# Kernel tuning notes

Measured on AMD Instinct MI355X. Metric: run time of the kernel, lower is better.

Reference implementation:

```python
import jax, jax.numpy as jnp
import numpy as np

B, T, C = 2, 2048, 1024
H = 16
HD = C // H  # head_size = 64
FF = 2 * C   # ffwd_size default = n_embd * 2
EPS = float(jnp.finfo(jnp.float32).eps)  # torch RMSNorm eps=None -> finfo eps


def rmsnorm(x, g):
    # torch.nn.RMSNorm: x / sqrt(mean(x^2) + eps) * weight
    ms = jnp.mean(jnp.square(x), axis=-1, keepdims=True)
    return x * jax.lax.rsqrt(ms + EPS) * g


def setup_inputs() -> dict:
    key = jax.random.key(0)
    ks = jax.random.split(key, 12)
    s_in = 1.0 / np.sqrt(C)
    s_ff = 1.0 / np.sqrt(FF)
    return {
        "target": jax.random.normal(ks[0], (B, T, C), dtype=jnp.float32),
        # per-head projections, torch Linear layout [out, in] stacked over heads: [H, HD, C]
        "wq": jax.random.uniform(ks[1], (H, HD, C), jnp.float32, -s_in, s_in),
        "wk": jax.random.uniform(ks[2], (H, HD, C), jnp.float32, -s_in, s_in),
        "wv": jax.random.uniform(ks[3], (H, HD, C), jnp.float32, -s_in, s_in),
        "w_proj": jax.random.uniform(ks[4], (C, H * HD), jnp.float32, -s_in, s_in),
        "b_proj": jax.random.uniform(ks[5], (C,), jnp.float32, -s_in, s_in),
        "w1": jax.random.uniform(ks[6], (FF, C), jnp.float32, -s_in, s_in),
        "b1": jax.random.uniform(ks[7], (FF,), jnp.float32, -s_in, s_in),
        "w2": jax.random.uniform(ks[8], (C, FF), jnp.float32, -s_ff, s_ff),
        "b2": jax.random.uniform(ks[9], (C,), jnp.float32, -s_ff, s_ff),
        "g1": jnp.ones((C,), jnp.float32),
        "g2": jnp.ones((C,), jnp.float32),
    }


def reference(target, wq, wk, wv, w_proj, b_proj, w1, b1, w2, b2, g1, g2):
    x = rmsnorm(target, g1)
    # q,k,v: [B,H,T,HD]
    q = jnp.einsum("btc,hdc->bhtd", x, wq)
    k = jnp.einsum("btc,hdc->bhtd", x, wk)
    v = jnp.einsum("btc,hdc->bhtd", x, wv)
    scale = HD ** -0.5
    wei = jnp.einsum("bhtd,bhsd->bhts", q, k) * scale  # [B,H,T,T]
    causal = jnp.tril(jnp.ones((T, T), dtype=bool))
    wei = jnp.where(causal, wei, -jnp.inf)
    wei = jax.nn.softmax(wei, axis=-1)
    attn = jnp.einsum("bhts,bhsd->bhtd", wei, v)  # [B,H,T,HD]
    attn = attn.transpose(0, 2, 1, 3).reshape(B, T, H * HD)  # concat heads
    attn = attn @ w_proj.T + b_proj
    target = target + attn
    y = rmsnorm(target, g2)
    h = jax.nn.gelu(y @ w1.T + b1, approximate=False)  # torch nn.GELU default = exact
    ff = h @ w2.T + b2
    return target + ff
```

## Files before the change

kernel.cpp:

```cpp
#include <hip/hip_runtime.h>
#include <math.h>

#define B_  2
#define T_  2048
#define C_  1024
#define H_  16
#define HD_ 64
#define FF_ 2048
#define EPS_ 1.1920929e-07f

typedef __attribute__((ext_vector_type(8))) short short8;
typedef __attribute__((ext_vector_type(4))) float f32x4;

__device__ __forceinline__ unsigned short f2bf(float f) {
    unsigned u = __float_as_uint(f);
    u += 0x7fffu + ((u >> 16) & 1u);
    return (unsigned short)(u >> 16);
}
__device__ __forceinline__ float bf2f(unsigned short u) {
    return __uint_as_float(((unsigned)u) << 16);
}

__global__ void prep_kernel(const float* __restrict__ wq, const float* __restrict__ wk,
                            const float* __restrict__ wv, const float* __restrict__ wp,
                            const float* __restrict__ w1, const float* __restrict__ w2,
                            unsigned short* __restrict__ wb,
                            const float* __restrict__ x, const float* __restrict__ g,
                            unsigned short* __restrict__ y) {
    int tid = threadIdx.x;
    if (blockIdx.x < 8192) {
        size_t i = ((size_t)blockIdx.x * 256 + tid) * 4;
        const float* src; size_t off = i;
        if      (i < 1048576u)  { src = wq; }
        else if (i < 2097152u)  { src = wk; off = i - 1048576u; }
        else if (i < 3145728u)  { src = wv; off = i - 2097152u; }
        else if (i < 4194304u)  { src = wp; off = i - 3145728u; }
        else if (i < 6291456u)  { src = w1; off = i - 4194304u; }
        else                    { src = w2; off = i - 6291456u; }
        float4 v4 = *(const float4*)(src + off);
        ushort4 o4;
        o4.x = f2bf(v4.x); o4.y = f2bf(v4.y); o4.z = f2bf(v4.z); o4.w = f2bf(v4.w);
        *(ushort4*)(wb + i) = o4;
    } else {
        int row = blockIdx.x - 8192;
        const float4* xr = (const float4*)(x + (size_t)row * C_);
        float4 xv = xr[tid];
        float ss = xv.x * xv.x + xv.y * xv.y + xv.z * xv.z + xv.w * xv.w;
        #pragma unroll
        for (int m = 32; m >= 1; m >>= 1) ss += __shfl_xor(ss, m, 64);
        __shared__ float sred[4];
        if ((tid & 63) == 0) sred[tid >> 6] = ss;
        __syncthreads();
        float tot = sred[0] + sred[1] + sred[2] + sred[3];
        float r = rsqrtf(tot * (1.0f / C_) + EPS_);
        float4 gv = ((const float4*)g)[tid];
        ushort4 o;
        o.x = f2bf(xv.x * r * gv.x);
        o.y = f2bf(xv.y * r * gv.y);
        o.z = f2bf(xv.z * r * gv.z);
        o.w = f2bf(xv.w * r * gv.w);
        *((ushort4*)(y + (size_t)row * C_) + tid) = o;
    }
}

__global__ void rmsnorm_bf16_kernel(const float* __restrict__ x, const float* __restrict__ g,
                                    unsigned short* __restrict__ y) {
    int row = blockIdx.x;
    int tid = threadIdx.x;
    const float4* xr = (const float4*)(x + (size_t)row * C_);
    float4 xv = xr[tid];
    float ss = xv.x * xv.x + xv.y * xv.y + xv.z * xv.z + xv.w * xv.w;
    #pragma unroll
    for (int m = 32; m >= 1; m >>= 1) ss += __shfl_xor(ss, m, 64);
    __shared__ float sred[4];
    if ((tid & 63) == 0) sred[tid >> 6] = ss;
    __syncthreads();
    float tot = sred[0] + sred[1] + sred[2] + sred[3];
    float r = rsqrtf(tot * (1.0f / C_) + EPS_);
    float4 gv = ((const float4*)g)[tid];
    ushort4 o;
    o.x = f2bf(xv.x * r * gv.x);
    o.y = f2bf(xv.y * r * gv.y);
    o.z = f2bf(xv.z * r * gv.z);
    o.w = f2bf(xv.w * r * gv.w);
    *((ushort4*)(y + (size_t)row * C_) + tid) = o;
}

template <int TM, int ACT, bool BIAS, bool RES, bool OBF16, int ROUTE>
__global__ __launch_bounds__(256) void mfma_gemm(
        const unsigned short* __restrict__ A, const unsigned short* __restrict__ W,
        const float* __restrict__ bias, const float* __restrict__ resid,
        void* __restrict__ O0, void* __restrict__ O1, void* __restrict__ O2,
        int M, int N, int K) {
    constexpr int ACH = TM / 8;
    constexpr int NCH = (ACH + 16) / 4;
    constexpr int MI  = TM / 32;
    __shared__ short As[2 * TM * 32];
    __shared__ short Bs[2 * 128 * 32];
    const int tid  = threadIdx.x;
    const int w    = tid >> 6, lane = tid & 63;
    const int tileN = blockIdx.x * 128, tileM = blockIdx.y * TM;

    const unsigned short* gsrc[NCH];
    short* ldst[NCH];
    #pragma unroll
    for (int i2 = 0; i2 < NCH; ++i2) {
        int c = w * NCH + i2;
        if (c < ACH) {
            int kh = c / (ACH / 2), lc = c % (ACH / 2);
            gsrc[i2] = A + (size_t)(tileM + lc * 16 + (lane >> 2)) * K + kh * 32 + (lane & 3) * 8;
            ldst[i2] = As + c * 512;
        } else {
            int c2 = c - ACH;
            int kh = c2 >> 3, lc = c2 & 7;
            gsrc[i2] = W + (size_t)(tileN + lc * 16 + (lane >> 2)) * K + kh * 32 + (lane & 3) * 8;
            ldst[i2] = Bs + c2 * 512;
        }
    }

    f32x4 acc[MI][4];
    const f32x4 zed = {0.f, 0.f, 0.f, 0.f};
    #pragma unroll
    for (int i = 0; i < MI; ++i)
        #pragma unroll
        for (int j = 0; j < 4; ++j) acc[i][j] = zed;

    const int wm = (w >> 1) * (TM / 2), wn = (w & 1) * 64;
    const int frow = lane & 15, koff = (lane >> 4) * 8;

    for (int k0 = 0; k0 < K; k0 += 64) {
        #pragma unroll
        for (int i2 = 0; i2 < NCH; ++i2)
            __builtin_amdgcn_global_load_lds(
                (const __attribute__((address_space(1))) unsigned*)(gsrc[i2] + k0),
                (__attribute__((address_space(3))) unsigned*)ldst[i2], 16, 0, 0);
        __syncthreads();

        #pragma unroll
        for (int kh = 0; kh < 2; ++kh) {
            short8 af[MI], bfr[4];
            #pragma unroll
            for (int i = 0; i < MI; ++i)
                af[i] = *(const short8*)(As + kh * TM * 32 + (wm + i * 16 + frow) * 32 + koff);
            #pragma unroll
            for (int j = 0; j < 4; ++j)
                bfr[j] = *(const short8*)(Bs + kh * 128 * 32 + (wn + j * 16 + frow) * 32 + koff);
            #pragma unroll
            for (int i = 0; i < MI; ++i)
                #pragma unroll
                for (int j = 0; j < 4; ++j)
                    acc[i][j] = __builtin_amdgcn_mfma_f32_16x16x32_bf16(af[i], bfr[j], acc[i][j], 0, 0, 0);
        }
        __syncthreads();
    }

    const int ecol = lane & 15, erow = (lane >> 4) * 4;
    const int zone = ROUTE ? (tileN >> 10) : 0;
    #pragma unroll
    for (int j = 0; j < 4; ++j) {
        int n = tileN + wn + j * 16 + ecol;
        float bv = BIAS ? bias[n] : 0.f;
        int nl = ROUTE ? (n & 1023) : n;
        #pragma unroll
        for (int i = 0; i < MI; ++i) {
            int mbase = tileM + wm + i * 16 + erow;
            #pragma unroll
            for (int r = 0; r < 4; ++r) {
                float val = acc[i][j][r] + bv;
                if (ACT == 1) val = 0.5f * val * (1.0f + erff(val * 0.70710678118654752f));
                int mrow = mbase + r;
                if (ROUTE) {
                    if (zone == 0) {
                        ((unsigned short*)O0)[(size_t)mrow * 1024 + nl] = f2bf(val * 0.18033688011112042f);
                    } else if (zone == 1) {
                        ((unsigned short*)O1)[(size_t)mrow * 1024 + nl] = f2bf(val);
                    } else {
                        int bb = mrow >> 11, tt = mrow & 2047;
                        int hh = nl >> 6, dd = nl & 63;
                        ((unsigned short*)O2)[((size_t)((bb * 16 + hh) * 64 + dd)) * 2048 + tt] = f2bf(val);
                    }
                } else {
                    size_t idx = (size_t)mrow * N + n;
                    if (RES) val += resid[idx];
                    if (OBF16) ((unsigned short*)O0)[idx] = f2bf(val);
                    else       ((float*)O0)[idx] = val;
                }
            }
        }
    }
}

__global__ __launch_bounds__(256) void flash_mfma_kernel(
        const unsigned short* __restrict__ q, const unsigned short* __restrict__ k,
        const unsigned short* __restrict__ vT, unsigned short* __restrict__ out) {
    __shared__ unsigned short KsA[64 * 64];
    __shared__ unsigned short VtA[64 * 64];
    __shared__ unsigned short KsB[64 * 64];
    __shared__ unsigned short VtB[64 * 64];
    __shared__ unsigned short Ps[2 * 4 * 16 * 40];

    const int tid  = threadIdx.x;
    const int w    = tid >> 6, lane = tid & 63;
    const int quad = lane >> 4, l15 = lane & 15;
    const int bh = blockIdx.x;
    const int qt = (gridDim.y - 1) - blockIdx.y;
    const int h = bh & (H_ - 1);
    const int b = bh >> 4;

    const size_t qkbase = (size_t)b * T_ * C_ + h * HD_;
    const size_t vbase  = (size_t)(b * H_ + h) * HD_ * T_;

    short8 QB[2];
    {
        const unsigned short* qp = q + qkbase + (size_t)(qt * 64 + w * 16 + l15) * C_;
        QB[0] = *(const short8*)(qp + quad * 8);
        QB[1] = *(const short8*)(qp + 32 + quad * 8);
    }

    f32x4 O[4];
    const f32x4 zed = {0.f, 0.f, 0.f, 0.f};
    #pragma unroll
    for (int dt = 0; dt < 4; ++dt) O[dt] = zed;
    float l_i = 0.f;

    const int qg = qt * 64 + w * 16 + l15;
    const int psoff = w * 640 + l15 * 40;
    const int r8 = lane >> 3, c7 = lane & 7;
    const int cswz = (c7 ^ r8) * 8;
    const int swz15 = (l15 & 7);

    auto stageKV = [&](unsigned short* Ksb, unsigned short* Vtb, int st_) {
        const int s0_ = st_ * 64;
        #pragma unroll
        for (int c = 0; c < 2; ++c) {
            const int row = w * 16 + c * 8 + r8;
            const unsigned short* gk = k + qkbase + (size_t)(s0_ + row) * C_ + cswz;
            __builtin_amdgcn_global_load_lds(
                (const __attribute__((address_space(1))) unsigned*)gk,
                (__attribute__((address_space(3))) unsigned*)(Ksb + (w * 16 + c * 8) * 64), 16, 0, 0);
            const unsigned short* gv = vT + vbase + (size_t)row * T_ + s0_ + cswz;
            __builtin_amdgcn_global_load_lds(
                (const __attribute__((address_space(1))) unsigned*)gv,
                (__attribute__((address_space(3))) unsigned*)(Vtb + (w * 16 + c * 8) * 64), 16, 0, 0);
        }
    };

    auto computeTile = [&](const unsigned short* Ksb, const unsigned short* Vtb, int st_) {
        const bool diag = (st_ == qt);
        const int s0_ = st_ * 64;
        #pragma unroll
        for (int sb = 0; sb < 2; ++sb) {
            const int sbl = sb * 32;
            f32x4 Sacc[2];
            #pragma unroll
            for (int u = 0; u < 2; ++u) {
                const int row = sbl + 16 * u + l15;
                const unsigned short* kr = Ksb + row * 64;
                const int kc = (quad ^ swz15) * 8;
                short8 KA0 = *(const short8*)(kr + kc);
                short8 KA1 = *(const short8*)(kr + (kc ^ 32));
                Sacc[u] = __builtin_amdgcn_mfma_f32_16x16x32_bf16(KA0, QB[0], zed, 0, 0, 0);
                Sacc[u] = __builtin_amdgcn_mfma_f32_16x16x32_bf16(KA1, QB[1], Sacc[u], 0, 0, 0);
            }
            float vals[8];
            if (diag) {
                #pragma unroll
                for (int u = 0; u < 2; ++u)
                    #pragma unroll
                    for (int r = 0; r < 4; ++r) {
                        int sg = s0_ + sbl + 16 * u + quad * 4 + r;
                        vals[u * 4 + r] = (sg > qg) ? 0.f : __builtin_amdgcn_exp2f(Sacc[u][r]);
                    }
            } else {
                #pragma unroll
                for (int u = 0; u < 2; ++u)
                    #pragma unroll
                    for (int r = 0; r < 4; ++r)
                        vals[u * 4 + r] = __builtin_amdgcn_exp2f(Sacc[u][r]);
            }
            float rs = 0.f;
            #pragma unroll
            for (int i = 0; i < 8; ++i) rs += vals[i];
            rs += __shfl_xor(rs, 16, 64);
            rs += __shfl_xor(rs, 32, 64);
            l_i += rs;

            #pragma unroll
            for (int u = 0; u < 2; ++u) {
                uint2 pw;
                pw.x = (unsigned)f2bf(vals[u * 4 + 0]) | ((unsigned)f2bf(vals[u * 4 + 1]) << 16);
                pw.y = (unsigned)f2bf(vals[u * 4 + 2]) | ((unsigned)f2bf(vals[u * 4 + 3]) << 16);
                *(uint2*)&Ps[sb * 2560 + psoff + 16 * u + quad * 4] = pw;
            }
            __builtin_amdgcn_sched_barrier(0);

            short8 PA = *(const short8*)&Ps[sb * 2560 + psoff + quad * 8];
            __builtin_amdgcn_s_setprio(1);
            #pragma unroll
            for (int dt = 0; dt < 4; ++dt) {
                const int vrow = 16 * dt + l15;
                short8 VB = *(const short8*)(Vtb + vrow * 64 + (((4 * sb + quad) ^ swz15) * 8));
                O[dt] = __builtin_amdgcn_mfma_f32_16x16x32_bf16(PA, VB, O[dt], 0, 0, 0);
            }
            __builtin_amdgcn_s_setprio(0);
        }
    };

    stageKV(KsA, VtA, 0);
    __syncthreads();
    int st = 0;
    for (;;) {
        if (st + 1 <= qt) stageKV(KsB, VtB, st + 1);
        computeTile(KsA, VtA, st);
        __syncthreads();
        ++st; if (st > qt) break;
        if (st + 1 <= qt) stageKV(KsA, VtA, st + 1);
        computeTile(KsB, VtB, st);
        __syncthreads();
        ++st; if (st > qt) break;
    }

    f32x4 inv;
    #pragma unroll
    for (int r = 0; r < 4; ++r) inv[r] = 1.0f / __shfl(l_i, quad * 4 + r, 64);
    #pragma unroll
    for (int dt = 0; dt < 4; ++dt)
        #pragma unroll
        for (int r = 0; r < 4; ++r) {
            int row = qt * 64 + w * 16 + quad * 4 + r;
            int col = h * HD_ + dt * 16 + l15;
            out[((size_t)(b * T_ + row)) * C_ + col] = f2bf(O[dt][r] * inv[r]);
        }
}

extern "C" void kernel_launch(void* const* d_in, const int* in_sizes, int n_in,
                              void* d_out, int out_size, void* d_ws, size_t ws_size,
                              hipStream_t stream) {
    const float* target = (const float*)d_in[0];
    const float* wq     = (const float*)d_in[1];
    const float* wk     = (const float*)d_in[2];
    const float* wv     = (const float*)d_in[3];
    const float* w_proj = (const float*)d_in[4];
    const float* b_proj = (const float*)d_in[5];
    const float* w1     = (const float*)d_in[6];
    const float* b1     = (const float*)d_in[7];
    const float* w2     = (const float*)d_in[8];
    const float* b2     = (const float*)d_in[9];
    const float* g1     = (const float*)d_in[10];
    const float* g2     = (const float*)d_in[11];
    float* out = (float*)d_out;

    char* ws = (char*)d_ws;
    const size_t MB = 1u << 20;
    unsigned short* xn = (unsigned short*)(ws);
    unsigned short* q  = (unsigned short*)(ws + 8 * MB);
    unsigned short* k  = (unsigned short*)(ws + 16 * MB);
    unsigned short* vt = (unsigned short*)(ws + 24 * MB);
    float*          x2 = (float*)(ws + 32 * MB);
    unsigned short* wb = (unsigned short*)(ws + 48 * MB);
    unsigned short* y  = q;
    unsigned short* hb = k;

    unsigned short* wqkv_b = wb;
    unsigned short* wp_b   = wb + 3145728u;
    unsigned short* w1_b   = wb + 4194304u;
    unsigned short* w2_b   = wb + 6291456u;

    const int M = B_ * T_;

    prep_kernel<<<12288, 256, 0, stream>>>(wq, wk, wv, w_proj, w1, w2, wb, target, g1, xn);

    mfma_gemm<128, 0, false, false, true, 1><<<dim3(24, M / 128), 256, 0, stream>>>(
        xn, wqkv_b, nullptr, nullptr, q, k, vt, M, 3072, C_);

    flash_mfma_kernel<<<dim3(B_ * H_, T_ / 64), 256, 0, stream>>>(q, k, vt, xn);

    mfma_gemm<64, 0, true, true, false, 0><<<dim3(C_ / 128, M / 64), 256, 0, stream>>>(
        xn, wp_b, b_proj, target, x2, nullptr, nullptr, M, C_, C_);

    rmsnorm_bf16_kernel<<<M, 256, 0, stream>>>(x2, g2, y);

    mfma_gemm<64, 1, true, false, true, 0><<<dim3(FF_ / 128, M / 64), 256, 0, stream>>>(
        y, w1_b, b1, nullptr, hb, nullptr, nullptr, M, FF_, C_);

    mfma_gemm<64, 0, true, true, false, 0><<<dim3(C_ / 128, M / 64), 256, 0, stream>>>(
        hb, w2_b, b2, x2, out, nullptr, nullptr, M, C_, FF_);
}
```

Baseline: 279.8 us.

## Pair causal query tiles per block and merge S-subblock compute in flash attention

Each attention block now processes two query tiles, a short one (pair) and a long one (31-pair), so every block does a balanced amount of causal work and the grid halves to 32x16. The per-tile compute is also restructured to compute all four 16-row score fragments before a single exp/rowsum/P-store pass, then issue eight PV MFMAs, removing the intra-tile sched_barrier split. This targets tail imbalance from the causal triangle and gives more ILP per tile. The cost is fewer blocks, hence lower occupancy across CUs, higher register pressure from 16 live score values, and a block that runs two tiles back to back.

```diff
diff --git a/kernel.cpp b/kernel.cpp
--- a/kernel.cpp
+++ b/kernel.cpp
@@ -203,7 +203,7 @@
     const int w    = tid >> 6, lane = tid & 63;
     const int quad = lane >> 4, l15 = lane & 15;
     const int bh = blockIdx.x;
-    const int qt = (gridDim.y - 1) - blockIdx.y;
+    const int pair = blockIdx.y;
     const int h = bh & (H_ - 1);
     const int b = bh >> 4;
 
@@ -211,23 +211,16 @@
     const size_t vbase  = (size_t)(b * H_ + h) * HD_ * T_;
 
     short8 QB[2];
-    {
-        const unsigned short* qp = q + qkbase + (size_t)(qt * 64 + w * 16 + l15) * C_;
-        QB[0] = *(const short8*)(qp + quad * 8);
-        QB[1] = *(const short8*)(qp + 32 + quad * 8);
-    }
-
     f32x4 O[4];
     const f32x4 zed = {0.f, 0.f, 0.f, 0.f};
-    #pragma unroll
-    for (int dt = 0; dt < 4; ++dt) O[dt] = zed;
     float l_i = 0.f;
-
-    const int qg = qt * 64 + w * 16 + l15;
+    int qt = 0, qg = 0;
+
     const int psoff = w * 640 + l15 * 40;
     const int r8 = lane >> 3, c7 = lane & 7;
     const int cswz = (c7 ^ r8) * 8;
     const int swz15 = (l15 & 7);
+    const int kc = (quad ^ swz15) * 8;
 
     auto stageKV = [&](unsigned short* Ksb, unsigned short* Vtb, int st_) {
         const int s0_ = st_ * 64;
@@ -248,89 +241,96 @@
     auto computeTile = [&](const unsigned short* Ksb, const unsigned short* Vtb, int st_) {
         const bool diag = (st_ == qt);
         const int s0_ = st_ * 64;
-        #pragma unroll
-        for (int sb = 0; sb < 2; ++sb) {
-            const int sbl = sb * 32;
-            f32x4 Sacc[2];
-            #pragma unroll
-            for (int u = 0; u < 2; ++u) {
-                const int row = sbl + 16 * u + l15;
-                const unsigned short* kr = Ksb + row * 64;
-                const int kc = (quad ^ swz15) * 8;
-                short8 KA0 = *(const short8*)(kr + kc);
-                short8 KA1 = *(const short8*)(kr + (kc ^ 32));
-                Sacc[u] = __builtin_amdgcn_mfma_f32_16x16x32_bf16(KA0, QB[0], zed, 0, 0, 0);
-                Sacc[u] = __builtin_amdgcn_mfma_f32_16x16x32_bf16(KA1, QB[1], Sacc[u], 0, 0, 0);
+        f32x4 Sacc[4];
+        #pragma unroll
+        for (int i = 0; i < 4; ++i) {
+            const unsigned short* kr = Ksb + (i * 16 + l15) * 64;
+            short8 KA0 = *(const short8*)(kr + kc);
+            short8 KA1 = *(const short8*)(kr + (kc ^ 32));
+            Sacc[i] = __builtin_amdgcn_mfma_f32_16x16x32_bf16(KA0, QB[0], zed, 0, 0, 0);
+            Sacc[i] = __builtin_amdgcn_mfma_f32_16x16x32_bf16(KA1, QB[1], Sacc[i], 0, 0, 0);
+        }
+        float vals[16];
+        #pragma unroll
+        for (int i = 0; i < 4; ++i)
+            #pragma unroll
+            for (int r = 0; r < 4; ++r) {
+                float e = __builtin_amdgcn_exp2f(Sacc[i][r]);
+                if (diag) {
+                    int sg = s0_ + i * 16 + quad * 4 + r;
+                    e = (sg > qg) ? 0.f : e;
+                }
+                vals[i * 4 + r] = e;
             }
-            float vals[8];
-            if (diag) {
-                #pragma unroll
-                for (int u = 0; u < 2; ++u)
-                    #pragma unroll
-                    for (int r = 0; r < 4; ++r) {
-                        int sg = s0_ + sbl + 16 * u + quad * 4 + r;
-                        vals[u * 4 + r] = (sg > qg) ? 0.f : __builtin_amdgcn_exp2f(Sacc[u][r]);
-                    }
-            } else {
-                #pragma unroll
-                for (int u = 0; u < 2; ++u)
-                    #pragma unroll
-                    for (int r = 0; r < 4; ++r)
-                        vals[u * 4 + r] = __builtin_amdgcn_exp2f(Sacc[u][r]);
+        float rs = 0.f;
+        #pragma unroll
+        for (int i = 0; i < 16; ++i) rs += vals[i];
+        rs += __shfl_xor(rs, 16, 64);
+        rs += __shfl_xor(rs, 32, 64);
+        l_i += rs;
+
+        #pragma unroll
+        for (int i = 0; i < 4; ++i) {
+            const int sb = i >> 1, u = i & 1;
+            uint2 pw;
+            pw.x = (unsigned)f2bf(vals[i * 4 + 0]) | ((unsigned)f2bf(vals[i * 4 + 1]) << 16);
+            pw.y = (unsigned)f2bf(vals[i * 4 + 2]) | ((unsigned)f2bf(vals[i * 4 + 3]) << 16);
+            *(uint2*)&Ps[sb * 2560 + psoff + 16 * u + quad * 4] = pw;
+        }
+
+        short8 PA0 = *(const short8*)&Ps[psoff + quad * 8];
+        short8 PA1 = *(const short8*)&Ps[2560 + psoff + quad * 8];
+        __builtin_amdgcn_s_setprio(1);
+        #pragma unroll
+        for (int dt = 0; dt < 4; ++dt) {
+            const unsigned short* vr = Vtb + (16 * dt + l15) * 64;
+            short8 VB0 = *(const short8*)(vr + ((quad ^ swz15) * 8));
+            short8 VB1 = *(const short8*)(vr + (((4 + quad) ^ swz15) * 8));
+            O[dt] = __builtin_amdgcn_mfma_f32_16x16x32_bf16(PA0, VB0, O[dt], 0, 0, 0);
+            O[dt] = __builtin_amdgcn_mfma_f32_16x16x32_bf16(PA1, VB1, O[dt], 0, 0, 0);
+        }
+        __builtin_amdgcn_s_setprio(0);
+    };
+
+    #pragma unroll 1
+    for (int half = 0; half < 2; ++half) {
+        qt = half ? (T_ / 64 - 1 - pair) : pair;
+        qg = qt * 64 + w * 16 + l15;
+        {
+            const unsigned short* qp = q + qkbase + (size_t)(qt * 64 + w * 16 + l15) * C_;
+            QB[0] = *(const short8*)(qp + quad * 8);
+            QB[1] = *(const short8*)(qp + 32 + quad * 8);
+        }
+        #pragma unroll
+        for (int dt = 0; dt < 4; ++dt) O[dt] = zed;
+        l_i = 0.f;
+
+        stageKV(KsA, VtA, 0);
+        __syncthreads();
+        int st = 0;
+        for (;;) {
+            if (st + 1 <= qt) stageKV(KsB, VtB, st + 1);
+            computeTile(KsA, VtA, st);
+            __syncthreads();
+            ++st; if (st > qt) break;
+            if (st + 1 <= qt) stageKV(KsA, VtA, st + 1);
+            computeTile(KsB, VtB, st);
+            __syncthreads();
+            ++st; if (st > qt) break;
+        }
+
+        f32x4 inv;
+        #pragma unroll
+        for (int r = 0; r < 4; ++r) inv[r] = 1.0f / __shfl(l_i, quad * 4 + r, 64);
+        #pragma unroll
+        for (int dt = 0; dt < 4; ++dt)
+            #pragma unroll
+            for (int r = 0; r < 4; ++r) {
+                int row = qt * 64 + w * 16 + quad * 4 + r;
+                int col = h * HD_ + dt * 16 + l15;
+                out[((size_t)(b * T_ + row)) * C_ + col] = f2bf(O[dt][r] * inv[r]);
             }
-            float rs = 0.f;
-            #pragma unroll
-            for (int i = 0; i < 8; ++i) rs += vals[i];
-            rs += __shfl_xor(rs, 16, 64);
-            rs += __shfl_xor(rs, 32, 64);
-            l_i += rs;
-
-            #pragma unroll
-            for (int u = 0; u < 2; ++u) {
-                uint2 pw;
-                pw.x = (unsigned)f2bf(vals[u * 4 + 0]) | ((unsigned)f2bf(vals[u * 4 + 1]) << 16);
-                pw.y = (unsigned)f2bf(vals[u * 4 + 2]) | ((unsigned)f2bf(vals[u * 4 + 3]) << 16);
-                *(uint2*)&Ps[sb * 2560 + psoff + 16 * u + quad * 4] = pw;
-            }
-            __builtin_amdgcn_sched_barrier(0);
-
-            short8 PA = *(const short8*)&Ps[sb * 2560 + psoff + quad * 8];
-            __builtin_amdgcn_s_setprio(1);
-            #pragma unroll
-            for (int dt = 0; dt < 4; ++dt) {
-                const int vrow = 16 * dt + l15;
-                short8 VB = *(const short8*)(Vtb + vrow * 64 + (((4 * sb + quad) ^ swz15) * 8));
-                O[dt] = __builtin_amdgcn_mfma_f32_16x16x32_bf16(PA, VB, O[dt], 0, 0, 0);
-            }
-            __builtin_amdgcn_s_setprio(0);
-        }
-    };
-
-    stageKV(KsA, VtA, 0);
-    __syncthreads();
-    int st = 0;
-    for (;;) {
-        if (st + 1 <= qt) stageKV(KsB, VtB, st + 1);
-        computeTile(KsA, VtA, st);
-        __syncthreads();
-        ++st; if (st > qt) break;
-        if (st + 1 <= qt) stageKV(KsA, VtA, st + 1);
-        computeTile(KsB, VtB, st);
-        __syncthreads();
-        ++st; if (st > qt) break;
-    }
-
-    f32x4 inv;
-    #pragma unroll
-    for (int r = 0; r < 4; ++r) inv[r] = 1.0f / __shfl(l_i, quad * 4 + r, 64);
-    #pragma unroll
-    for (int dt = 0; dt < 4; ++dt)
-        #pragma unroll
-        for (int r = 0; r < 4; ++r) {
-            int row = qt * 64 + w * 16 + quad * 4 + r;
-            int col = h * HD_ + dt * 16 + l15;
-            out[((size_t)(b * T_ + row)) * C_ + col] = f2bf(O[dt][r] * inv[r]);
-        }
+    }
 }
 
 extern "C" void kernel_launch(void* const* d_in, const int* in_sizes, int n_in,
@@ -373,7 +373,7 @@
     mfma_gemm<128, 0, false, false, true, 1><<<dim3(24, M / 128), 256, 0, stream>>>(
         xn, wqkv_b, nullptr, nullptr, q, k, vt, M, 3072, C_);
 
-    flash_mfma_kernel<<<dim3(B_ * H_, T_ / 64), 256, 0, stream>>>(q, k, vt, xn);
+    flash_mfma_kernel<<<dim3(B_ * H_, T_ / 128), 256, 0, stream>>>(q, k, vt, xn);
 
     mfma_gemm<64, 0, true, true, false, 0><<<dim3(C_ / 128, M / 64), 256, 0, stream>>>(
         xn, wp_b, b_proj, target, x2, nullptr, nullptr, M, C_, C_);
```

Result: slower. 285.5 us (+2.0%).
